# Optimization experiments

Measured on AMD Instinct MI355X. Metric: run time of the kernel, lower is better.

The kernel has to match this reference:

```python
import jax, jax.numpy as jnp
import numpy as np

N = 100000      # num graph nodes
E = 1600000     # num edges (avg degree 16)
IN = 128        # in_channels
H = 128         # hidden_channels
B = 4096        # query batch
CTX = 20        # context set length (indices[:, 3:])


def setup_inputs() -> dict:
    key = jax.random.key(0)
    ks = jax.random.split(key, 16)
    inp = {
        "indices": jax.random.randint(ks[0], (B, 3 + CTX), 0, N, dtype=jnp.int64),
        "src": jax.random.randint(ks[1], (E,), 0, N, dtype=jnp.int32),
        "dst": jax.random.randint(ks[2], (E,), 0, N, dtype=jnp.int32),
        "w": jax.random.uniform(ks[3], (E,), dtype=jnp.float32),
        # learned params
        "ndata": jax.random.normal(ks[4], (N, IN), dtype=jnp.float32),
        "W1": jax.random.normal(ks[5], (H, IN), dtype=jnp.float32) * (1.0 / np.sqrt(IN)),
        "b1": jnp.zeros((H,), jnp.float32),
        "W2": jax.random.normal(ks[6], (H, H), dtype=jnp.float32) * (1.0 / np.sqrt(H)),
        "b2": jnp.zeros((H,), jnp.float32),
        "eps": jnp.zeros((2,), jnp.float32),  # learn_eps, one per GINConv
        "Wc1": jax.random.normal(ks[7], (H, 3 * H), dtype=jnp.float32) * (1.0 / np.sqrt(3 * H)),
        "bc1": jnp.zeros((H,), jnp.float32),
        "Wc2": jax.random.normal(ks[8], (H // 2, H), dtype=jnp.float32) * (1.0 / np.sqrt(H)),
        "bc2": jnp.zeros((H // 2,), jnp.float32),
        "Wc3": jax.random.normal(ks[9], (1, H // 2), dtype=jnp.float32) * (1.0 / np.sqrt(H // 2)),
        "bc3": jnp.zeros((1,), jnp.float32),
    }
    return inp


def _gin_conv(x, src, dst, w, deg, eps, W, b):
    # DGL GINConv(mean, learn_eps): h = lin((1+eps)*x + mean_{in-edges}(w_e * x_src))
    msg = w[:, None] * x[src]                                   # [E, D]
    agg = jax.ops.segment_sum(msg, dst, num_segments=N) / deg   # [N, D]
    return ((1.0 + eps) * x + agg) @ W.T + b


def reference(indices, src, dst, w, ndata, W1, b1, W2, b2, eps,
              Wc1, bc1, Wc2, bc2, Wc3, bc3):
    deg = jax.ops.segment_sum(jnp.ones((E,), ndata.dtype), dst, num_segments=N)
    deg = jnp.maximum(deg, 1.0)[:, None]

    x = ndata
    x = jax.nn.relu(_gin_conv(x, src, dst, w, deg, eps[0], W1, b1))  # dropout inactive (eval)
    x = _gin_conv(x, src, dst, w, deg, eps[1], W2, b2)               # last layer: no relu
    x = x.at[0].set(0.0)                                             # x[0] = zeros

    ing1 = x[indices[:, 0]]   # [B, H]
    ing2 = x[indices[:, 1]]   # [B, H]

    # embed_context: mean over nonzero-index context members
    ctx_idx = indices[:, 3:]                                   # [B, CTX]
    ctx_sum = x[ctx_idx].sum(axis=1)                           # [B, H]
    norm = jnp.maximum((ctx_idx > 0).sum(axis=1), 1).astype(x.dtype)[:, None]
    ctx = ctx_sum / norm

    y = jnp.concatenate([ing1, ing2, ctx], axis=1)             # [B, 3H]
    y = jax.nn.relu(y @ Wc1.T + bc1)
    y = jax.nn.relu(y @ Wc2.T + bc2)
    y = y @ Wc3.T + bc3                                        # [B, 1]
    return y
```

## Files before the change

### kernel.cpp

```cpp
#include <hip/hip_runtime.h>
#include <hip/hip_fp16.h>


#define CONV_NPB 32
#define FIN_EPB 8

struct __align__(8)  h4 { __half2 a, b; };
struct __align__(16) h8 { __half2 a, b, c, d; };

__device__ __forceinline__ float4 h4f(h4 u) {
  return make_float4(__low2float(u.a), __high2float(u.a),
                     __low2float(u.b), __high2float(u.b));
}
__device__ __forceinline__ h4 f4h(float4 v) {
  h4 u; u.a = __floats2half2_rn(v.x, v.y); u.b = __floats2half2_rn(v.z, v.w);
  return u;
}

__global__ void init_kernel(const float* __restrict__ W1, const float* __restrict__ W2,
                            const float* __restrict__ Wc1, const float* __restrict__ Wc2,
                            const float* __restrict__ ndata, __half* __restrict__ xh0,
                            float* __restrict__ Wt1, float* __restrict__ Wt2,
                            float* __restrict__ Wc1t, float* __restrict__ Wc2t,
                            int* __restrict__ cnt, int n) {
  int i = blockIdx.x * blockDim.x + threadIdx.x;
  if (i < n) cnt[i] = 0;
  const int cbase = i * 8;
  if (cbase < n * 128) {
    const float4 v0 = *(const float4*)&ndata[cbase];
    const float4 v1 = *(const float4*)&ndata[cbase + 4];
    h8 u;
    u.a = __floats2half2_rn(v0.x, v0.y);
    u.b = __floats2half2_rn(v0.z, v0.w);
    u.c = __floats2half2_rn(v1.x, v1.y);
    u.d = __floats2half2_rn(v1.z, v1.w);
    *(h8*)&xh0[cbase] = u;
  }
  if (i < 16384) {
    int f = i >> 7, k = i & 127;
    Wt1[k * 128 + f] = W1[i];
  } else if (i < 32768) {
    int j = i - 16384; int f = j >> 7, k = j & 127;
    Wt2[k * 128 + f] = W2[j];
  } else if (i < 81920) {
    int j = i - 32768; int f = j / 384, k = j % 384;
    Wc1t[k * 128 + f] = Wc1[j];
  } else if (i < 90112) {
    int j = i - 81920; int f = j >> 7, k = j & 127;
    Wc2t[k * 64 + f] = Wc2[j];
  }
}

__global__ void hist_kernel(const int* __restrict__ dst, int* __restrict__ cnt,
                            int* __restrict__ rank, int E) {
  int e = (blockIdx.x * blockDim.x + threadIdx.x) * 4;
  if (e + 3 < E) {
    const int4 d = *(const int4*)&dst[e];
    int4 r;
    r.x = atomicAdd(&cnt[d.x], 1);
    r.y = atomicAdd(&cnt[d.y], 1);
    r.z = atomicAdd(&cnt[d.z], 1);
    r.w = atomicAdd(&cnt[d.w], 1);
    *(int4*)&rank[e] = r;
  } else {
    for (; e < E; ++e) rank[e] = atomicAdd(&cnt[dst[e]], 1);
  }
}

__global__ void scan1_kernel(const int* __restrict__ cnt, int* __restrict__ prow,
                             int* __restrict__ bsum, int n) {
  __shared__ int smem[256];
  const int t = threadIdx.x;
  const int base = blockIdx.x * 2048 + t * 8;
  int v[8];
  int s = 0;
#pragma unroll
  for (int j = 0; j < 8; ++j) {
    int idx = base + j;
    v[j] = (idx < n) ? ((cnt[idx] + 7) & ~7) : 0;
    s += v[j];
  }
  smem[t] = s;
  __syncthreads();
  for (int off = 1; off < 256; off <<= 1) {
    int add = (t >= off) ? smem[t - off] : 0;
    __syncthreads();
    smem[t] += add;
    __syncthreads();
  }
  int run = smem[t] - s;
  if (t == 255) bsum[blockIdx.x] = smem[255];
#pragma unroll
  for (int j = 0; j < 8; ++j) {
    int idx = base + j;
    if (idx < n) prow[idx] = run;
    run += v[j];
  }
}

__global__ void scan2_kernel(int* __restrict__ bsum, int nb) {
  const int t = threadIdx.x;
  if (nb <= 64) {
    const int orig = (t < nb) ? bsum[t] : 0;
    int v = orig;
#pragma unroll
    for (int off = 1; off < 64; off <<= 1) {
      int u = __shfl_up(v, off);
      if (t >= off) v += u;
    }
    if (t == nb - 1) bsum[nb] = v;
    if (t < nb) bsum[t] = v - orig;
  } else if (t == 0) {
    int run = 0;
    for (int i = 0; i < nb; ++i) { int v = bsum[i]; bsum[i] = run; run += v; }
    bsum[nb] = run;
  }
}

__global__ void scatter_kernel(const int* __restrict__ src, const int* __restrict__ dst,
                               const float* __restrict__ w, const int* __restrict__ prow,
                               const int* __restrict__ bsum, const int* __restrict__ rank,
                               const int* __restrict__ cnt,
                               int2* __restrict__ epack, int E, int n) {
  const int i = blockIdx.x * blockDim.x + threadIdx.x;
  int e = i * 4;
  if (e + 3 < E) {
    const int4 d = *(const int4*)&dst[e];
    const int4 s = *(const int4*)&src[e];
    const float4 wv = *(const float4*)&w[e];
    const int4 r = *(const int4*)&rank[e];
    epack[prow[d.x] + bsum[d.x >> 11] + r.x] = make_int2(s.x, __float_as_int(wv.x));
    epack[prow[d.y] + bsum[d.y >> 11] + r.y] = make_int2(s.y, __float_as_int(wv.y));
    epack[prow[d.z] + bsum[d.z >> 11] + r.z] = make_int2(s.z, __float_as_int(wv.z));
    epack[prow[d.w] + bsum[d.w >> 11] + r.w] = make_int2(s.w, __float_as_int(wv.w));
  } else {
    for (; e < E; ++e) {
      const int d = dst[e];
      epack[prow[d] + bsum[d >> 11] + rank[e]] = make_int2(src[e], __float_as_int(w[e]));
    }
  }
  if (i < n) {
    const int c = cnt[i];
    const int start = prow[i] + bsum[i >> 11] + c;
    const int pc = ((c + 7) & ~7) - c;
    for (int j = 0; j < pc; ++j) epack[start + j] = make_int2(0, 0);
  }
}

__launch_bounds__(256, 8)
__global__ void conv_kernel(const float* __restrict__ xin, const __half* __restrict__ xinh,
                            float* __restrict__ xout, __half* __restrict__ xouth,
                            const int* __restrict__ prow, const int* __restrict__ bsum,
                            const int* __restrict__ cnt,
                            const int2* __restrict__ epack,
                            const float* __restrict__ Wt,
                            const float* __restrict__ bias, const float* __restrict__ eps,
                            int epsidx, int dorelu, int zerorow0, int writef32,
                            int n, int nchunk) {
  __shared__ float xm[CONV_NPB * 128];
  __shared__ int rp_s[CONV_NPB + 1];
  const int t = threadIdx.x;
  const int nb = blockIdx.x * CONV_NPB;
  const float epsv = 1.0f + eps[epsidx];

#pragma unroll
  for (int i = 0; i < 4; ++i)
    *(float4*)&xm[(t + i * 256) * 4] = make_float4(0.f, 0.f, 0.f, 0.f);
  if (t <= CONV_NPB) {
    const int node = nb + t;
    rp_s[t] = (node >= n) ? bsum[nchunk] : (prow[node] + bsum[node >> 11]);
  }
  __syncthreads();

  {
    const int L = t >> 5;
    const int lane = t & 31;
    const int f0 = lane * 4;
    const int e0 = rp_s[0], eT = rp_s[CONV_NPB];
    const int nbat = (eT - e0) >> 3;
    const int chunk = (((nbat + 7) >> 3)) << 3;
    const int jb = e0 + L * chunk;
    const int je = min(jb + chunk, eT);
    if (jb < je) {
      const int4* ep4 = (const int4*)epack;
      int r = 0;
      while (rp_s[r + 1] <= jb) ++r;
      float4 acc = make_float4(0.f, 0.f, 0.f, 0.f);
      int h = jb >> 1;
      int4 q0 = ep4[h + 0];
      int4 q1 = ep4[h + 1];
      int4 q2 = ep4[h + 2];
      int4 q3 = ep4[h + 3];
      for (int j = jb; j < je; j += 8) {
        if (rp_s[r + 1] <= j) {
          float* bp = &xm[r * 128 + lane];
          atomicAdd(bp + 0,  acc.x);
          atomicAdd(bp + 32, acc.y);
          atomicAdd(bp + 64, acc.z);
          atomicAdd(bp + 96, acc.w);
          acc = make_float4(0.f, 0.f, 0.f, 0.f);
          do { ++r; } while (rp_s[r + 1] <= j);
        }
        const h4 u0 = *(const h4*)&xinh[(size_t)q0.x * 128 + f0];
        const h4 u1 = *(const h4*)&xinh[(size_t)q0.z * 128 + f0];
        const h4 u2 = *(const h4*)&xinh[(size_t)q1.x * 128 + f0];
        const h4 u3 = *(const h4*)&xinh[(size_t)q1.z * 128 + f0];
        const h4 u4 = *(const h4*)&xinh[(size_t)q2.x * 128 + f0];
        const h4 u5 = *(const h4*)&xinh[(size_t)q2.z * 128 + f0];
        const h4 u6 = *(const h4*)&xinh[(size_t)q3.x * 128 + f0];
        const h4 u7 = *(const h4*)&xinh[(size_t)q3.z * 128 + f0];
        const float w0 = __int_as_float(q0.y), w1 = __int_as_float(q0.w);
        const float w2 = __int_as_float(q1.y), w3 = __int_as_float(q1.w);
        const float w4 = __int_as_float(q2.y), w5 = __int_as_float(q2.w);
        const float w6 = __int_as_float(q3.y), w7 = __int_as_float(q3.w);
        const int jn = (j + 8 < je) ? (j + 8) : j;
        const int hn = jn >> 1;
        q0 = ep4[hn + 0];
        q1 = ep4[hn + 1];
        q2 = ep4[hn + 2];
        q3 = ep4[hn + 3];
        const float4 a0 = h4f(u0), a1 = h4f(u1), a2 = h4f(u2), a3 = h4f(u3);
        const float4 a4 = h4f(u4), a5 = h4f(u5), a6 = h4f(u6), a7 = h4f(u7);
        acc.x += w0 * a0.x + w1 * a1.x + w2 * a2.x + w3 * a3.x
               + w4 * a4.x + w5 * a5.x + w6 * a6.x + w7 * a7.x;
        acc.y += w0 * a0.y + w1 * a1.y + w2 * a2.y + w3 * a3.y
               + w4 * a4.y + w5 * a5.y + w6 * a6.y + w7 * a7.y;
        acc.z += w0 * a0.z + w1 * a1.z + w2 * a2.z + w3 * a3.z
               + w4 * a4.z + w5 * a5.z + w6 * a6.z + w7 * a7.z;
        acc.w += w0 * a0.w + w1 * a1.w + w2 * a2.w + w3 * a3.w
               + w4 * a4.w + w5 * a5.w + w6 * a6.w + w7 * a7.w;
      }
      float* bp = &xm[r * 128 + lane];
      atomicAdd(bp + 0,  acc.x);
      atomicAdd(bp + 32, acc.y);
      atomicAdd(bp + 64, acc.z);
      atomicAdd(bp + 96, acc.w);
    }
  }
  __syncthreads();

  {
    float4 m[4];
#pragma unroll
    for (int q = 0; q < 4; ++q) {
      const int task = t + q * 256;
      const int r = task >> 5;
      const int fg = task & 31;
      m[q].x = xm[r * 128 + fg];
      m[q].y = xm[r * 128 + 32 + fg];
      m[q].z = xm[r * 128 + 64 + fg];
      m[q].w = xm[r * 128 + 96 + fg];
    }
    __syncthreads();
#pragma unroll
    for (int q = 0; q < 4; ++q) {
      const int task = t + q * 256;
      const int r = task >> 5;
      const int fg = task & 31;
      const int f0 = fg * 4;
      const int node = nb + r;
      float4 v = make_float4(0.f, 0.f, 0.f, 0.f);
      if (node < n) {
        const int d = cnt[node];
        const float rdeg = 1.0f / (float)(d > 1 ? d : 1);
        const float4 xv = *(const float4*)&xin[(size_t)node * 128 + f0];
        v.x = epsv * xv.x + m[q].x * rdeg;
        v.y = epsv * xv.y + m[q].y * rdeg;
        v.z = epsv * xv.z + m[q].z * rdeg;
        v.w = epsv * xv.w + m[q].w * rdeg;
      }
      *(float4*)&xm[r * 128 + f0] = v;
    }
  }
  __syncthreads();

  {
    const int fg = t & 31;
    const int rg = t >> 5;
    const int f0 = fg * 4;
    const int r0 = rg * 4;
    float4 acc[4];
#pragma unroll
    for (int r = 0; r < 4; ++r) acc[r] = make_float4(0.f, 0.f, 0.f, 0.f);
    for (int k = 0; k < 128; k += 4) {
      const float4 w0 = *(const float4*)&Wt[(k + 0) * 128 + f0];
      const float4 w1 = *(const float4*)&Wt[(k + 1) * 128 + f0];
      const float4 w2 = *(const float4*)&Wt[(k + 2) * 128 + f0];
      const float4 w3 = *(const float4*)&Wt[(k + 3) * 128 + f0];
#pragma unroll
      for (int r = 0; r < 4; ++r) {
        const float4 xv = *(const float4*)&xm[(r0 + r) * 128 + k];
        acc[r].x += xv.x * w0.x + xv.y * w1.x + xv.z * w2.x + xv.w * w3.x;
        acc[r].y += xv.x * w0.y + xv.y * w1.y + xv.z * w2.y + xv.w * w3.y;
        acc[r].z += xv.x * w0.z + xv.y * w1.z + xv.z * w2.z + xv.w * w3.z;
        acc[r].w += xv.x * w0.w + xv.y * w1.w + xv.z * w2.w + xv.w * w3.w;
      }
    }
    const float4 bv = *(const float4*)&bias[f0];
#pragma unroll
    for (int r = 0; r < 4; ++r) {
      const int node = nb + r0 + r;
      if (node < n) {
        float4 v;
        v.x = acc[r].x + bv.x;
        v.y = acc[r].y + bv.y;
        v.z = acc[r].z + bv.z;
        v.w = acc[r].w + bv.w;
        if (dorelu) {
          v.x = fmaxf(v.x, 0.f); v.y = fmaxf(v.y, 0.f);
          v.z = fmaxf(v.z, 0.f); v.w = fmaxf(v.w, 0.f);
        }
        if (zerorow0 && node == 0) { v.x = 0.f; v.y = 0.f; v.z = 0.f; v.w = 0.f; }
        *(h4*)&xouth[(size_t)node * 128 + f0] = f4h(v);
        if (writef32) *(float4*)&xout[(size_t)node * 128 + f0] = v;
      }
    }
  }
}

__launch_bounds__(256, 4)
__global__ void final_kernel(const __half* __restrict__ x2h, const int* __restrict__ indices,
                             const float* __restrict__ Wc1t, const float* __restrict__ bc1,
                             const float* __restrict__ Wc2t, const float* __restrict__ bc2,
                             const float* __restrict__ Wc3, const float* __restrict__ bc3,
                             float* __restrict__ out) {
  __shared__ float ysm[FIN_EPB * 384];
  __shared__ float h1s[FIN_EPB * 128];
  __shared__ float h2s[FIN_EPB * 64];
  __shared__ int ind_s[FIN_EPB * 23];
  __shared__ float ccs[FIN_EPB];
  const int t = threadIdx.x;
  const int b0 = blockIdx.x * FIN_EPB;

  if (t < FIN_EPB * 23) ind_s[t] = indices[(size_t)b0 * 23 + t];
  __syncthreads();
  if (t < FIN_EPB) {
    int cc = 0;
#pragma unroll
    for (int j = 0; j < 20; ++j) cc += (ind_s[t * 23 + 3 + j] > 0) ? 1 : 0;
    ccs[t] = 1.0f / (float)(cc > 0 ? cc : 1);
  }
  __syncthreads();

  {
#pragma unroll
    for (int q = 0; q < 2; ++q) {
      const int s = t + q * 256;
      const int e = s >> 6;
      const int hf = (s >> 5) & 1;
      const int fg = s & 31;
      const int idx = ind_s[e * 23 + hf];
      const h4 u = *(const h4*)&x2h[(size_t)idx * 128 + fg * 4];
      *(float4*)&ysm[e * 384 + hf * 128 + fg * 4] = h4f(u);
    }
    const int e = t >> 5;
    const int fg = t & 31;
    float4 acc = make_float4(0.f, 0.f, 0.f, 0.f);
#pragma unroll
    for (int j = 0; j < 20; ++j) {
      const int cj = ind_s[e * 23 + 3 + j];
      const h4 u = *(const h4*)&x2h[(size_t)cj * 128 + fg * 4];
      const float4 a = h4f(u);
      acc.x += a.x; acc.y += a.y; acc.z += a.z; acc.w += a.w;
    }
    const float sc = ccs[e];
    acc.x *= sc; acc.y *= sc; acc.z *= sc; acc.w *= sc;
    *(float4*)&ysm[e * 384 + 256 + fg * 4] = acc;
  }
  __syncthreads();

  {
    const int f1 = t & 127;
    const int eh = t >> 7;
    float acc[4];
    const float b = bc1[f1];
#pragma unroll
    for (int i = 0; i < 4; ++i) acc[i] = b;
    for (int k = 0; k < 384; k += 4) {
      const float wv0 = Wc1t[(k + 0) * 128 + f1];
      const float wv1 = Wc1t[(k + 1) * 128 + f1];
      const float wv2 = Wc1t[(k + 2) * 128 + f1];
      const float wv3 = Wc1t[(k + 3) * 128 + f1];
#pragma unroll
      for (int i = 0; i < 4; ++i) {
        const float4 yv = *(const float4*)&ysm[(eh * 4 + i) * 384 + k];
        acc[i] += yv.x * wv0 + yv.y * wv1 + yv.z * wv2 + yv.w * wv3;
      }
    }
#pragma unroll
    for (int i = 0; i < 4; ++i)
      h1s[(eh * 4 + i) * 128 + f1] = fmaxf(acc[i], 0.f);
  }
  __syncthreads();

  {
    const int f2 = t & 63;
    const int eg = t >> 6;
    float acc[2];
    const float b = bc2[f2];
#pragma unroll
    for (int i = 0; i < 2; ++i) acc[i] = b;
    for (int k = 0; k < 128; k += 4) {
      const float wv0 = Wc2t[(k + 0) * 64 + f2];
      const float wv1 = Wc2t[(k + 1) * 64 + f2];
      const float wv2 = Wc2t[(k + 2) * 64 + f2];
      const float wv3 = Wc2t[(k + 3) * 64 + f2];
#pragma unroll
      for (int i = 0; i < 2; ++i) {
        const float4 hv = *(const float4*)&h1s[(eg * 2 + i) * 128 + k];
        acc[i] += hv.x * wv0 + hv.y * wv1 + hv.z * wv2 + hv.w * wv3;
      }
    }
#pragma unroll
    for (int i = 0; i < 2; ++i)
      h2s[(eg * 2 + i) * 64 + f2] = fmaxf(acc[i], 0.f);
  }
  __syncthreads();

  {
    const int e = t >> 5;
    const int l = t & 31;
    float p = h2s[e * 64 + l] * Wc3[l] + h2s[e * 64 + l + 32] * Wc3[l + 32];
#pragma unroll
    for (int o = 16; o > 0; o >>= 1) p += __shfl_down(p, o, 32);
    if (l == 0) out[b0 + e] = p + bc3[0];
  }
}

extern "C" void kernel_launch(void* const* d_in, const int* in_sizes, int n_in,
                              void* d_out, int out_size, void* d_ws, size_t ws_size,
                              hipStream_t stream) {
  const int* indices = (const int*)d_in[0];
  const int* src = (const int*)d_in[1];
  const int* dst = (const int*)d_in[2];
  const float* w = (const float*)d_in[3];
  const float* ndata = (const float*)d_in[4];
  const float* W1 = (const float*)d_in[5];
  const float* b1 = (const float*)d_in[6];
  const float* W2 = (const float*)d_in[7];
  const float* b2 = (const float*)d_in[8];
  const float* eps = (const float*)d_in[9];
  const float* Wc1 = (const float*)d_in[10];
  const float* bc1 = (const float*)d_in[11];
  const float* Wc2 = (const float*)d_in[12];
  const float* bc2 = (const float*)d_in[13];
  const float* Wc3 = (const float*)d_in[14];
  const float* bc3 = (const float*)d_in[15];
  float* out = (float*)d_out;

  const int E = in_sizes[1];
  const int N = in_sizes[4] / 128;
  const int B = in_sizes[0] / 23;

  char* ws = (char*)d_ws;
  size_t off = 0;
  auto alloc = [&](size_t bytes) -> char* {
    char* p = ws + off;
    off = (off + bytes + 255) & ~(size_t)255;
    return p;
  };
  const size_t Epad = (size_t)E + 8 * (size_t)N;
  int* cnt = (int*)alloc((size_t)N * 4);
  int* prow = (int*)alloc((size_t)(N + 1) * 4);
  int* rank = (int*)alloc((size_t)E * 4);
  int* bsum = (int*)alloc(256 * 4);
  int2* epack = (int2*)alloc(Epad * 8);
  float* x1 = (float*)alloc((size_t)N * 128 * 4);
  __half* xh0 = (__half*)alloc((size_t)N * 128 * 2);
  __half* x1h = (__half*)alloc((size_t)N * 128 * 2);
  float* Wt1 = (float*)alloc(16384 * 4);
  float* Wt2 = (float*)alloc(16384 * 4);
  float* Wc1t = (float*)alloc(49152 * 4);
  float* Wc2t = (float*)alloc(8192 * 4);
  __half* x2h = xh0;

  const int ncast = (N * 128 + 7) / 8;
  int ninit = (N > 90112) ? N : 90112;
  if (ncast > ninit) ninit = ncast;
  init_kernel<<<(ninit + 255) / 256, 256, 0, stream>>>(W1, W2, Wc1, Wc2, ndata, xh0,
                                                       Wt1, Wt2, Wc1t, Wc2t, cnt, N);
  const int Eq = (E + 3) / 4;
  hist_kernel<<<(Eq + 255) / 256, 256, 0, stream>>>(dst, cnt, rank, E);
  const int nchunk = (N + 2047) / 2048;
  scan1_kernel<<<nchunk, 256, 0, stream>>>(cnt, prow, bsum, N);
  scan2_kernel<<<1, 64, 0, stream>>>(bsum, nchunk);
  const int nsc = (Eq > N) ? Eq : N;
  scatter_kernel<<<(nsc + 255) / 256, 256, 0, stream>>>(src, dst, w, prow, bsum, rank, cnt, epack, E, N);

  const int nconv = (N + CONV_NPB - 1) / CONV_NPB;
  conv_kernel<<<nconv, 256, 0, stream>>>(ndata, xh0, x1, x1h, prow, bsum, cnt, epack,
                                         Wt1, b1, eps, 0, 1, 0, 1, N, nchunk);
  conv_kernel<<<nconv, 256, 0, stream>>>(x1, x1h, nullptr, x2h, prow, bsum, cnt, epack,
                                         Wt2, b2, eps, 1, 0, 1, 0, N, nchunk);

  final_kernel<<<B / FIN_EPB, 256, 0, stream>>>(x2h, indices, Wc1t, bc1, Wc2t, bc2, Wc3, bc3, out);
}
```

Baseline: 513.7 us.

## Restructure edge gather to wave-level superblocks with 16-byte per-lane loads

Reworks the neighbor-aggregation loop so each 64-lane wave handles a contiguous range of 8-edge superblocks. Each 16-lane group gathers a different edge's full 128-feature row with 16-byte half8 loads, and edge descriptors are fetched at a wave-uniform address (readfirstlane) with double-buffered prefetch. Accumulator layout changes to contiguous 8 features per lane, which removes the strided readback stage and one barrier. The intent is fewer, wider memory requests and better latency hiding. In exchange it costs more registers and LDS atomics, since four groups write to the same row.

Result: slower. 999.2 us (+94.5%).

```diff
diff --git a/kernel.cpp b/kernel.cpp
--- a/kernel.cpp
+++ b/kernel.cpp
@@ -16,6 +16,14 @@
   h4 u; u.a = __floats2half2_rn(v.x, v.y); u.b = __floats2half2_rn(v.z, v.w);
   return u;
 }
+__device__ __forceinline__ void fma8(float (&ac)[8], h8 u, float w) {
+  ac[0] += w * __low2float(u.a);  ac[1] += w * __high2float(u.a);
+  ac[2] += w * __low2float(u.b);  ac[3] += w * __high2float(u.b);
+  ac[4] += w * __low2float(u.c);  ac[5] += w * __high2float(u.c);
+  ac[6] += w * __low2float(u.d);  ac[7] += w * __high2float(u.d);
+}
+
+#define SEL4(g, a, b, c, d) ((g) < 2 ? ((g) == 0 ? (a) : (b)) : ((g) == 2 ? (c) : (d)))
 
 __global__ void init_kernel(const float* __restrict__ W1, const float* __restrict__ W2,
                             const float* __restrict__ Wc1, const float* __restrict__ Wc2,
@@ -173,85 +181,86 @@
   __syncthreads();
 
   {
-    const int L = t >> 5;
-    const int lane = t & 31;
-    const int f0 = lane * 4;
+    const int lane = t & 63;
+    const int wv = t >> 6;
+    const int grp = lane >> 4;
+    const int fl = lane & 15;
     const int e0 = rp_s[0], eT = rp_s[CONV_NPB];
-    const int nbat = (eT - e0) >> 3;
-    const int chunk = (((nbat + 7) >> 3)) << 3;
-    const int jb = e0 + L * chunk;
-    const int je = min(jb + chunk, eT);
-    if (jb < je) {
-      const int4* ep4 = (const int4*)epack;
+    const int sbT = (eT - e0) >> 3;
+    const int csb = (sbT + 3) >> 2;
+    const int sw0 = wv * csb;
+    const int send = min(sw0 + csb, sbT);
+    if (sw0 < send) {
+      const int* epi = (const int*)epack;
+      const int sbase = e0 >> 3;
+      float acc[8];
+#pragma unroll
+      for (int c = 0; c < 8; ++c) acc[c] = 0.f;
+      int dvA[16], dvB[16];
+      h8 gA0, gA1, gB0, gB1;
+      float wA0, wA1, wB0, wB1;
+
+#define LOADDESC(dv, si) do {                                            \
+        const int _db = __builtin_amdgcn_readfirstlane(sbase + (si)) << 4; \
+        _Pragma("unroll")                                                \
+        for (int _k = 0; _k < 16; ++_k) (dv)[_k] = epi[_db + _k];        \
+      } while (0)
+
+#define ISSUEG(dv, g0, g1, ww0, ww1) do {                                \
+        const int _s0 = SEL4(grp, (dv)[0], (dv)[2], (dv)[4], (dv)[6]);   \
+        const int _s1 = SEL4(grp, (dv)[8], (dv)[10], (dv)[12], (dv)[14]);\
+        (ww0) = __int_as_float(SEL4(grp, (dv)[1], (dv)[3], (dv)[5], (dv)[7]));   \
+        (ww1) = __int_as_float(SEL4(grp, (dv)[9], (dv)[11], (dv)[13], (dv)[15]));\
+        (g0) = *(const h8*)&xinh[(size_t)_s0 * 128 + fl * 8];            \
+        (g1) = *(const h8*)&xinh[(size_t)_s1 * 128 + fl * 8];            \
+      } while (0)
+
+#define FLUSHACC(rr) do {                                                \
+        float* _bp = &xm[(rr) * 128 + fl * 8];                           \
+        _Pragma("unroll")                                                \
+        for (int _c = 0; _c < 8; ++_c) {                                 \
+          atomicAdd(_bp + _c, acc[_c]); acc[_c] = 0.f;                   \
+        }                                                                \
+      } while (0)
+
+      LOADDESC(dvA, sw0);
+      ISSUEG(dvA, gA0, gA1, wA0, wA1);
+      if (sw0 + 1 < send) LOADDESC(dvB, sw0 + 1);
       int r = 0;
-      while (rp_s[r + 1] <= jb) ++r;
-      float4 acc = make_float4(0.f, 0.f, 0.f, 0.f);
-      int h = jb >> 1;
-      int4 q0 = ep4[h + 0];
-      int4 q1 = ep4[h + 1];
-      int4 q2 = ep4[h + 2];
-      int4 q3 = ep4[h + 3];
-      for (int j = jb; j < je; j += 8) {
-        if (rp_s[r + 1] <= j) {
-          float* bp = &xm[r * 128 + lane];
-          atomicAdd(bp + 0,  acc.x);
-          atomicAdd(bp + 32, acc.y);
-          atomicAdd(bp + 64, acc.z);
-          atomicAdd(bp + 96, acc.w);
-          acc = make_float4(0.f, 0.f, 0.f, 0.f);
-          do { ++r; } while (rp_s[r + 1] <= j);
+      for (int i = sw0; i < send; i += 2) {
+        const bool hasB = (i + 1 < send);
+        if (hasB) ISSUEG(dvB, gB0, gB1, wB0, wB1);
+        if (i + 2 < send) LOADDESC(dvA, i + 2);
+        {
+          const int j = e0 + 8 * i;
+          int rn = r;
+          while (rp_s[rn + 1] <= j) ++rn;
+          if (rn != r) { FLUSHACC(r); r = rn; }
         }
-        const h4 u0 = *(const h4*)&xinh[(size_t)q0.x * 128 + f0];
-        const h4 u1 = *(const h4*)&xinh[(size_t)q0.z * 128 + f0];
-        const h4 u2 = *(const h4*)&xinh[(size_t)q1.x * 128 + f0];
-        const h4 u3 = *(const h4*)&xinh[(size_t)q1.z * 128 + f0];
-        const h4 u4 = *(const h4*)&xinh[(size_t)q2.x * 128 + f0];
-        const h4 u5 = *(const h4*)&xinh[(size_t)q2.z * 128 + f0];
-        const h4 u6 = *(const h4*)&xinh[(size_t)q3.x * 128 + f0];
-        const h4 u7 = *(const h4*)&xinh[(size_t)q3.z * 128 + f0];
-        const float w0 = __int_as_float(q0.y), w1 = __int_as_float(q0.w);
-        const float w2 = __int_as_float(q1.y), w3 = __int_as_float(q1.w);
-        const float w4 = __int_as_float(q2.y), w5 = __int_as_float(q2.w);
-        const float w6 = __int_as_float(q3.y), w7 = __int_as_float(q3.w);
-        const int jn = (j + 8 < je) ? (j + 8) : j;
-        const int hn = jn >> 1;
-        q0 = ep4[hn + 0];
-        q1 = ep4[hn + 1];
-        q2 = ep4[hn + 2];
-        q3 = ep4[hn + 3];
-        const float4 a0 = h4f(u0), a1 = h4f(u1), a2 = h4f(u2), a3 = h4f(u3);
-        const float4 a4 = h4f(u4), a5 = h4f(u5), a6 = h4f(u6), a7 = h4f(u7);
-        acc.x += w0 * a0.x + w1 * a1.x + w2 * a2.x + w3 * a3.x
-               + w4 * a4.x + w5 * a5.x + w6 * a6.x + w7 * a7.x;
-        acc.y += w0 * a0.y + w1 * a1.y + w2 * a2.y + w3 * a3.y
-               + w4 * a4.y + w5 * a5.y + w6 * a6.y + w7 * a7.y;
-        acc.z += w0 * a0.z + w1 * a1.z + w2 * a2.z + w3 * a3.z
-               + w4 * a4.z + w5 * a5.z + w6 * a6.z + w7 * a7.z;
-        acc.w += w0 * a0.w + w1 * a1.w + w2 * a2.w + w3 * a3.w
-               + w4 * a4.w + w5 * a5.w + w6 * a6.w + w7 * a7.w;
+        fma8(acc, gA0, wA0);
+        fma8(acc, gA1, wA1);
+        if (hasB) {
+          if (i + 2 < send) ISSUEG(dvA, gA0, gA1, wA0, wA1);
+          if (i + 3 < send) LOADDESC(dvB, i + 3);
+          {
+            const int j = e0 + 8 * (i + 1);
+            int rn = r;
+            while (rp_s[rn + 1] <= j) ++rn;
+            if (rn != r) { FLUSHACC(r); r = rn; }
+          }
+          fma8(acc, gB0, wB0);
+          fma8(acc, gB1, wB1);
+        }
       }
-      float* bp = &xm[r * 128 + lane];
-      atomicAdd(bp + 0,  acc.x);
-      atomicAdd(bp + 32, acc.y);
-      atomicAdd(bp + 64, acc.z);
-      atomicAdd(bp + 96, acc.w);
-    }
-  }
-  __syncthreads();
-
-  {
-    float4 m[4];
-#pragma unroll
-    for (int q = 0; q < 4; ++q) {
-      const int task = t + q * 256;
-      const int r = task >> 5;
-      const int fg = task & 31;
-      m[q].x = xm[r * 128 + fg];
-      m[q].y = xm[r * 128 + 32 + fg];
-      m[q].z = xm[r * 128 + 64 + fg];
-      m[q].w = xm[r * 128 + 96 + fg];
-    }
-    __syncthreads();
+      FLUSHACC(r);
+#undef LOADDESC
+#undef ISSUEG
+#undef FLUSHACC
+    }
+  }
+  __syncthreads();
+
+  {
 #pragma unroll
     for (int q = 0; q < 4; ++q) {
       const int task = t + q * 256;
@@ -264,10 +273,11 @@
         const int d = cnt[node];
         const float rdeg = 1.0f / (float)(d > 1 ? d : 1);
         const float4 xv = *(const float4*)&xin[(size_t)node * 128 + f0];
-        v.x = epsv * xv.x + m[q].x * rdeg;
-        v.y = epsv * xv.y + m[q].y * rdeg;
-        v.z = epsv * xv.z + m[q].z * rdeg;
-        v.w = epsv * xv.w + m[q].w * rdeg;
+        const float4 m = *(const float4*)&xm[r * 128 + f0];
+        v.x = epsv * xv.x + m.x * rdeg;
+        v.y = epsv * xv.y + m.y * rdeg;
+        v.z = epsv * xv.z + m.z * rdeg;
+        v.w = epsv * xv.w + m.w * rdeg;
       }
       *(float4*)&xm[r * 128 + f0] = v;
     }
```
